# Kernel tuning notes

Measured on AMD Instinct MI355X. Metric: run time of the kernel, lower is better.

The kernel has to match this reference:

```python
import jax, jax.numpy as jnp
import numpy as np

TOPK = 8  # n_activated_experts


def setup_inputs() -> dict:
    key = jax.random.key(0)
    k1, k2 = jax.random.split(key)
    tokens, dim, n_experts = 8192, 4096, 64
    x = jax.random.normal(k1, (tokens, dim), dtype=jnp.float32)
    weight = jax.random.normal(k2, (n_experts, dim), dtype=jnp.float32) * 0.02
    bias = jnp.zeros((n_experts,), dtype=jnp.float32)
    return {"x": x, "weight": weight, "bias": bias}


def reference(x, weight, bias):
    # scores: [tokens, n_experts]
    scores = jnp.einsum("td,ed->te", x, weight) + bias
    probs = jax.nn.softmax(scores, axis=-1)  # score_func == 'softmax'
    weights, indices = jax.lax.top_k(probs, TOPK)
    return probs, indices
```

## Files before the change

### kernel.cpp

```cpp
#include <hip/hip_runtime.h>
#include <math.h>

#define DIM     4096
#define NEXP    64
#define TOPK_N  8
#define TAU     2.0e-4f
#define TGB     64
#define KC      512
#define NKC     (DIM / KC)
#define KS32    (KC / 32)

#define WS_WHI_OFF  0
#define WS_WLO_OFF  (512*1024)
#define WS_PART_OFF (1024*1024)

typedef __attribute__((ext_vector_type(8))) short short8;
typedef __attribute__((ext_vector_type(4))) float f32x4;

#define WALL __builtin_amdgcn_sched_barrier(0)

__device__ __forceinline__ void cvt8(float4 a0, float4 a1, short8& hv, short8& lv) {
    float f[8] = {a0.x, a0.y, a0.z, a0.w, a1.x, a1.y, a1.z, a1.w};
    union { short8 v; unsigned u[4]; } H, L;
    #pragma unroll
    for (int i = 0; i < 4; ++i) {
        unsigned b0 = __float_as_uint(f[2*i]);
        unsigned b1 = __float_as_uint(f[2*i+1]);
        float r0 = f[2*i]   - __uint_as_float(b0 & 0xffff0000u);
        float r1 = f[2*i+1] - __uint_as_float(b1 & 0xffff0000u);
        H.u[i] = (b0 >> 16) | (b1 & 0xffff0000u);
        L.u[i] = (__float_as_uint(r0) >> 16) | (__float_as_uint(r1) & 0xffff0000u);
    }
    hv = H.v; lv = L.v;
}

__global__ __launch_bounds__(256, 4)
void cvt_w_kernel(const float* __restrict__ w, unsigned short* __restrict__ whi,
                  unsigned short* __restrict__ wlo) {
    const int g = blockIdx.x * 256 + threadIdx.x;
    const float* p = w + (size_t)g * 8;
    union { short8 v; uint4 q; } H, L;
    float4 a0 = *(const float4*)(p);
    float4 a1 = *(const float4*)(p + 4);
    cvt8(a0, a1, H.v, L.v);
    *(uint4*)(whi + (size_t)g * 8) = H.q;
    *(uint4*)(wlo + (size_t)g * 8) = L.q;
}

__global__ __launch_bounds__(256, 4)
void zero_kernel(float* __restrict__ p) {
    const size_t g = (size_t)blockIdx.x * 256 + threadIdx.x;
    *(float4*)(p + g * 4) = (float4){0.f, 0.f, 0.f, 0.f};
}

template<int USE_PART>
__global__ __launch_bounds__(256, 4)
void gemm_part_kernel(const float* __restrict__ x, const unsigned short* __restrict__ whi,
                      const unsigned short* __restrict__ wlo, float* __restrict__ dst,
                      int ntok) {
    const int tid  = threadIdx.x;
    const int lane = tid & 63;
    const int wvm  = tid >> 6;
    const int nl   = lane & 15;
    const int q    = lane >> 4;
    const int kc   = blockIdx.x & (NKC - 1);
    const int tg   = blockIdx.x >> 3;
    const int t0   = tg * TGB + wvm * 16;
    const int k0   = kc * KC;

    const float* xr = x + (size_t)(t0 + nl) * DIM + k0;
    const unsigned short* bh[4];
    const unsigned short* bl[4];
    #pragma unroll
    for (int nf = 0; nf < 4; ++nf) {
        const size_t o = (size_t)(nf * 16 + nl) * DIM + k0;
        bh[nf] = whi + o;
        bl[nf] = wlo + o;
    }

    f32x4 acc[4];
    #pragma unroll
    for (int nf = 0; nf < 4; ++nf) acc[nf] = (f32x4){0.f, 0.f, 0.f, 0.f};

    float4 Ar[2][2];
    Ar[0][0] = *(const float4*)(xr + q * 8);
    Ar[0][1] = *(const float4*)(xr + q * 8 + 4);

    #pragma unroll 2
    for (int s = 0; s < KS32; ++s) {
        const int buf = s & 1;
        if (s + 1 < KS32) {
            const int kk = (s + 1) * 32 + q * 8;
            Ar[buf ^ 1][0] = *(const float4*)(xr + kk);
            Ar[buf ^ 1][1] = *(const float4*)(xr + kk + 4);
        }
        WALL;
        const int kk = s * 32 + q * 8;
        short8 bhv[4], blv[4];
        #pragma unroll
        for (int nf = 0; nf < 4; ++nf) {
            bhv[nf] = *(const short8*)(bh[nf] + kk);
            blv[nf] = *(const short8*)(bl[nf] + kk);
        }
        short8 ahi, alo;
        cvt8(Ar[buf][0], Ar[buf][1], ahi, alo);
        #pragma unroll
        for (int nf = 0; nf < 4; ++nf) {
            acc[nf] = __builtin_amdgcn_mfma_f32_16x16x32_bf16(ahi, blv[nf], acc[nf], 0, 0, 0);
            acc[nf] = __builtin_amdgcn_mfma_f32_16x16x32_bf16(alo, bhv[nf], acc[nf], 0, 0, 0);
            acc[nf] = __builtin_amdgcn_mfma_f32_16x16x32_bf16(ahi, bhv[nf], acc[nf], 0, 0, 0);
        }
        WALL;
    }

    #pragma unroll
    for (int nf = 0; nf < 4; ++nf)
        #pragma unroll
        for (int r = 0; r < 4; ++r) {
            const int tok = t0 + q * 4 + r;
            const int e   = nf * 16 + nl;
            if (USE_PART)
                dst[((size_t)tok * NKC + kc) * NEXP + e] = acc[nf][r];
            else
                atomicAdd(&dst[(size_t)tok * NEXP + e], acc[nf][r]);
        }
}

template<int USE_PART>
__global__ __launch_bounds__(256, 4)
void finish_kernel(const float* __restrict__ src, const float* __restrict__ bias,
                   const float* __restrict__ x, const float* __restrict__ wfp,
                   float* __restrict__ out, int ntok) {
    __shared__ float lds_s[4][68];
    __shared__ float t9[4][12];

    const int tid  = threadIdx.x;
    const int lane = tid & 63;
    const int wv   = tid >> 6;
    const int tok  = blockIdx.x * 4 + wv;

    float s;
    if (USE_PART) {
        const float* pr = src + (size_t)tok * NKC * NEXP;
        s = pr[lane];
        #pragma unroll
        for (int c = 1; c < NKC; ++c) s += pr[c * NEXP + lane];
    } else {
        s = src[(size_t)tok * NEXP + lane];
    }
    s += bias[lane];

    float m = s;
    #pragma unroll
    for (int off = 32; off > 0; off >>= 1)
        m = fmaxf(m, __shfl_xor(m, off, 64));
    const float ex = expf(s - m);
    float sum = ex;
    #pragma unroll
    for (int off = 32; off > 0; off >>= 1)
        sum += __shfl_xor(sum, off, 64);
    out[(size_t)tok * NEXP + lane] = ex / sum;

    lds_s[wv][lane] = s;
    int rank = 0;
    #pragma unroll
    for (int i = 0; i < 16; ++i) {
        const float4 v4 = *(const float4*)(&lds_s[wv][i * 4]);
        rank += (int)((v4.x > s) || (v4.x == s && (i * 4 + 0) < lane));
        rank += (int)((v4.y > s) || (v4.y == s && (i * 4 + 1) < lane));
        rank += (int)((v4.z > s) || (v4.z == s && (i * 4 + 2) < lane));
        rank += (int)((v4.w > s) || (v4.w == s && (i * 4 + 3) < lane));
    }
    float* __restrict__ out_idx = out + (size_t)ntok * NEXP;
    if (rank < TOPK_N + 1) t9[wv][rank] = s;
    if (rank < TOPK_N)
        out_idx[(size_t)tok * TOPK_N + rank] = (float)lane;

    float gap = 1e30f;
    if (lane < TOPK_N) gap = t9[wv][lane] - t9[wv][lane + 1];
    if (__any(gap < TAU)) {
        const float thr = t9[wv][TOPK_N] - TAU;
        const unsigned long long cmask = __ballot(s >= thr);
        double dscv = -1.0e300;
        unsigned long long mm = cmask;
        while (mm) {
            const int e = __builtin_ctzll(mm);
            mm &= mm - 1;
            const float* wr  = wfp + (size_t)e * DIM;
            const float* xrr = x + (size_t)tok * DIM;
            double a = 0.0;
            #pragma unroll 4
            for (int kk = 0; kk < 16; ++kk) {
                const int k = kk * 256 + lane * 4;
                const float4 wv4 = *(const float4*)(wr + k);
                const float4 xv  = *(const float4*)(xrr + k);
                a = fma((double)xv.x, (double)wv4.x, a);
                a = fma((double)xv.y, (double)wv4.y, a);
                a = fma((double)xv.z, (double)wv4.z, a);
                a = fma((double)xv.w, (double)wv4.w, a);
            }
            #pragma unroll
            for (int off = 32; off > 0; off >>= 1)
                a += __shfl_xor(a, off, 64);
            a += (double)bias[e];
            if (lane == e) dscv = a;
        }
        double cv = dscv;
        for (int r = 0; r < TOPK_N; ++r) {
            double bv = cv;
            int    bi = lane;
            #pragma unroll
            for (int off = 32; off > 0; off >>= 1) {
                const double ov = __shfl_xor(bv, off, 64);
                const int    oi = __shfl_xor(bi, off, 64);
                if (ov > bv || (ov == bv && oi < bi)) { bv = ov; bi = oi; }
            }
            if (lane == r)
                out_idx[(size_t)tok * TOPK_N + r] = (float)bi;
            if (lane == bi) cv = -1.0e301;
        }
    }
}

extern "C" void kernel_launch(void* const* d_in, const int* in_sizes, int n_in,
                              void* d_out, int out_size, void* d_ws, size_t ws_size,
                              hipStream_t stream) {
    const float* x  = (const float*)d_in[0];
    const float* w  = (const float*)d_in[1];
    const float* bs = (const float*)d_in[2];
    float* out = (float*)d_out;

    unsigned short* whi = (unsigned short*)((char*)d_ws + WS_WHI_OFF);
    unsigned short* wlo = (unsigned short*)((char*)d_ws + WS_WLO_OFF);

    const int ntok = in_sizes[0] / DIM;

    hipLaunchKernelGGL(cvt_w_kernel, dim3((NEXP * DIM) / 8 / 256), dim3(256), 0, stream,
                       w, whi, wlo);

    const size_t part_need = (size_t)WS_PART_OFF + (size_t)ntok * NKC * NEXP * sizeof(float);
    if (ws_size >= part_need) {
        float* part = (float*)((char*)d_ws + WS_PART_OFF);
        hipLaunchKernelGGL((gemm_part_kernel<1>), dim3((ntok / TGB) * NKC), dim3(256), 0, stream,
                           x, whi, wlo, part, ntok);
        hipLaunchKernelGGL((finish_kernel<1>), dim3(ntok / 4), dim3(256), 0, stream,
                           part, bs, x, w, out, ntok);
    } else {
        hipLaunchKernelGGL(zero_kernel, dim3((ntok * NEXP) / 1024), dim3(256), 0, stream, out);
        hipLaunchKernelGGL((gemm_part_kernel<0>), dim3((ntok / TGB) * NKC), dim3(256), 0, stream,
                           x, whi, wlo, out, ntok);
        hipLaunchKernelGGL((finish_kernel<0>), dim3(ntok / 4), dim3(256), 0, stream,
                           out, bs, x, w, out, ntok);
    }
}
```

Baseline: 263.0 us.

## Stage A and B tiles through swizzled LDS with async global-to-LDS loads

The GEMM kernel now stages the x and weight (hi/lo bf16) tiles into double-buffered shared memory using global_load_lds direct transfers, with an XOR swizzle to avoid bank conflicts. Before, each wave loaded its A and B fragments straight from global memory into registers. The intent is to share weight tiles across the block's waves and overlap the next stage's loads with the current stage's MFMA work. In exchange it adds a block-wide barrier every stage and uses more LDS, which may reduce occupancy.

```diff
diff --git a/kernel.cpp b/kernel.cpp
--- a/kernel.cpp
+++ b/kernel.cpp
@@ -8,7 +8,7 @@
 #define TGB     64
 #define KC      512
 #define NKC     (DIM / KC)
-#define KS32    (KC / 32)
+#define NST     (KC / 32)
 
 #define WS_WHI_OFF  0
 #define WS_WLO_OFF  (512*1024)
@@ -32,6 +32,12 @@
         L.u[i] = (__float_as_uint(r0) >> 16) | (__float_as_uint(r1) & 0xffff0000u);
     }
     hv = H.v; lv = L.v;
+}
+
+__device__ __forceinline__ void async16(void* lds, const void* g) {
+    __builtin_amdgcn_global_load_lds(
+        (const __attribute__((address_space(1))) unsigned int*)g,
+        (__attribute__((address_space(3))) unsigned int*)lds, 16, 0, 0);
 }
 
 __global__ __launch_bounds__(256, 4)
@@ -58,66 +64,88 @@
 void gemm_part_kernel(const float* __restrict__ x, const unsigned short* __restrict__ whi,
                       const unsigned short* __restrict__ wlo, float* __restrict__ dst,
                       int ntok) {
+    __shared__ float          A_lds[2][TGB][32];
+    __shared__ unsigned short B_lds[2][NEXP][64];
+
     const int tid  = threadIdx.x;
     const int lane = tid & 63;
-    const int wvm  = tid >> 6;
+    const int wv   = tid >> 6;
     const int nl   = lane & 15;
     const int q    = lane >> 4;
     const int kc   = blockIdx.x & (NKC - 1);
     const int tg   = blockIdx.x >> 3;
-    const int t0   = tg * TGB + wvm * 16;
+    const int t0b  = tg * TGB;
     const int k0   = kc * KC;
 
-    const float* xr = x + (size_t)(t0 + nl) * DIM + k0;
-    const unsigned short* bh[4];
-    const unsigned short* bl[4];
-    #pragma unroll
-    for (int nf = 0; nf < 4; ++nf) {
-        const size_t o = (size_t)(nf * 16 + nl) * DIM + k0;
-        bh[nf] = whi + o;
-        bl[nf] = wlo + o;
+    int arow[2], brow[2];
+    const float* gA[2];
+    const unsigned short* gB[2];
+    #pragma unroll
+    for (int i = 0; i < 2; ++i) {
+        const int inst = wv * 2 + i;
+        {
+            const int r   = inst * 8 + (lane >> 3);
+            const int scb = ((lane & 7) * 16) ^ ((r & 7) << 4);
+            arow[i] = inst * 8;
+            gA[i] = x + (size_t)(t0b + r) * DIM + k0 + (scb >> 2);
+        }
+        {
+            const int e   = inst * 8 + (lane >> 3);
+            const int scb = ((lane & 7) * 16) ^ ((e & 7) << 4);
+            brow[i] = inst * 8;
+            const unsigned short* base = (scb & 64) ? wlo : whi;
+            gB[i] = base + (size_t)e * DIM + k0 + ((scb & 63) >> 1);
+        }
     }
 
     f32x4 acc[4];
     #pragma unroll
     for (int nf = 0; nf < 4; ++nf) acc[nf] = (f32x4){0.f, 0.f, 0.f, 0.f};
 
-    float4 Ar[2][2];
-    Ar[0][0] = *(const float4*)(xr + q * 8);
-    Ar[0][1] = *(const float4*)(xr + q * 8 + 4);
-
+#define STAGE(b_, st_) do {                                                    \
+        async16(&A_lds[b_][arow[0]][0], gA[0] + (st_) * 32);                   \
+        async16(&A_lds[b_][arow[1]][0], gA[1] + (st_) * 32);                   \
+        async16(&B_lds[b_][brow[0]][0], gB[0] + (st_) * 32);                   \
+        async16(&B_lds[b_][brow[1]][0], gB[1] + (st_) * 32);                   \
+    } while (0)
+
+#define COMPUTE(b_) do {                                                       \
+        const char* Ab_ = (const char*)&A_lds[b_][wv * 16 + nl][0];            \
+        const int swz_ = (nl & 7) << 4;                                        \
+        float4 a0_ = *(const float4*)(Ab_ + ((q * 32) ^ swz_));                \
+        float4 a1_ = *(const float4*)(Ab_ + ((q * 32 + 16) ^ swz_));           \
+        short8 ahi_, alo_;                                                     \
+        cvt8(a0_, a1_, ahi_, alo_);                                            \
+        _Pragma("unroll")                                                      \
+        for (int nf_ = 0; nf_ < 4; ++nf_) {                                    \
+            const char* Bb_ = (const char*)&B_lds[b_][nf_ * 16 + nl][0];       \
+            short8 bh_ = *(const short8*)(Bb_ + ((q * 16) ^ swz_));            \
+            short8 bl_ = *(const short8*)(Bb_ + ((64 + q * 16) ^ swz_));       \
+            acc[nf_] = __builtin_amdgcn_mfma_f32_16x16x32_bf16(ahi_, bl_, acc[nf_], 0, 0, 0); \
+            acc[nf_] = __builtin_amdgcn_mfma_f32_16x16x32_bf16(alo_, bh_, acc[nf_], 0, 0, 0); \
+            acc[nf_] = __builtin_amdgcn_mfma_f32_16x16x32_bf16(ahi_, bh_, acc[nf_], 0, 0, 0); \
+        }                                                                      \
+    } while (0)
+
+    STAGE(0, 0);
+    __syncthreads();
     #pragma unroll 2
-    for (int s = 0; s < KS32; ++s) {
-        const int buf = s & 1;
-        if (s + 1 < KS32) {
-            const int kk = (s + 1) * 32 + q * 8;
-            Ar[buf ^ 1][0] = *(const float4*)(xr + kk);
-            Ar[buf ^ 1][1] = *(const float4*)(xr + kk + 4);
-        }
+    for (int st = 0; st < NST; ++st) {
+        const int b = st & 1;
+        if (st + 1 < NST) STAGE(b ^ 1, st + 1);
         WALL;
-        const int kk = s * 32 + q * 8;
-        short8 bhv[4], blv[4];
-        #pragma unroll
-        for (int nf = 0; nf < 4; ++nf) {
-            bhv[nf] = *(const short8*)(bh[nf] + kk);
-            blv[nf] = *(const short8*)(bl[nf] + kk);
-        }
-        short8 ahi, alo;
-        cvt8(Ar[buf][0], Ar[buf][1], ahi, alo);
-        #pragma unroll
-        for (int nf = 0; nf < 4; ++nf) {
-            acc[nf] = __builtin_amdgcn_mfma_f32_16x16x32_bf16(ahi, blv[nf], acc[nf], 0, 0, 0);
-            acc[nf] = __builtin_amdgcn_mfma_f32_16x16x32_bf16(alo, bhv[nf], acc[nf], 0, 0, 0);
-            acc[nf] = __builtin_amdgcn_mfma_f32_16x16x32_bf16(ahi, bhv[nf], acc[nf], 0, 0, 0);
-        }
-        WALL;
-    }
+        COMPUTE(b);
+        __syncthreads();
+    }
+
+#undef STAGE
+#undef COMPUTE
 
     #pragma unroll
     for (int nf = 0; nf < 4; ++nf)
         #pragma unroll
         for (int r = 0; r < 4; ++r) {
-            const int tok = t0 + q * 4 + r;
+            const int tok = t0b + wv * 16 + q * 4 + r;
             const int e   = nf * 16 + nl;
             if (USE_PART)
                 dst[((size_t)tok * NKC + kc) * NEXP + e] = acc[nf][r];
```

Result: faster. 228.4 us (-13.2%).
